# Optimization experiments

Hardware: AMD Instinct MI355X
Metric: run time of the kernel (lower is better)

Reference implementation:

```python
import jax, jax.numpy as jnp
import numpy as np

B, N = 16384, 32
OBS0, OBS1, OBS2 = 16, 64, 16
D = 64          # hidden dim / single_head_dim
H = 3           # n_heads
NACT = 2


def setup_inputs() -> dict:
    key = jax.random.key(0)
    ks = jax.random.split(key, 32)
    w = lambda i, shape: jax.random.normal(ks[i], shape, jnp.float32) * 0.05
    return {
        "s0": jax.random.normal(ks[0], (B, OBS0), jnp.float32),
        "s1": jax.random.normal(ks[1], (B, OBS1), jnp.float32),
        "s2": jax.random.normal(ks[2], (B, N, OBS2), jnp.float32),
        "W_own": w(3, (D, OBS0)), "b_own": w(4, (D,)),
        "W_env": w(5, (D, OBS1)), "b_env": w(6, (D,)),
        "W_s1": w(7, (D, OBS2)), "b_s1": w(8, (D,)),
        "W_s2": w(9, (D, D)),    "b_s2": w(10, (D,)),
        "W_q": w(11, (D, D)), "W_k": w(12, (D, D)), "W_v": w(13, (D, D)),
        "W_cq": w(14, (D, D)), "W_ck": w(15, (D, D)), "W_cv": w(16, (D, D)),
        "W_mo": w(17, (128, H * D)), "b_mo": w(18, (128,)),
        "W_a1": w(19, (64, 128)), "b_a1": w(20, (64,)),
        "W_a2": w(21, (NACT, 64)), "b_a2": w(22, (NACT,)),
    }


def reference(s0, s1, s2, W_own, b_own, W_env, b_env, W_s1, b_s1, W_s2, b_s2,
              W_q, W_k, W_v, W_cq, W_ck, W_cv, W_mo, b_mo, W_a1, b_a1, W_a2, b_a2):
    # branch encoders
    own_e = jax.nn.relu(s0 @ W_own.T + b_own)            # [B, 64]
    env_e = jax.nn.relu(s1 @ W_env.T + b_env)            # [B, 64]
    h = jax.nn.relu(s2 @ W_s1.T + b_s1)                  # [B, N, 64]
    intru_e = jax.nn.relu(h @ W_s2.T + b_s2)             # [B, N, 64]

    # masked single-head attention pooling over neighbors
    q = own_e @ W_q.T                                    # [B, 64]
    k = intru_e @ W_k.T                                  # [B, N, 64]
    v = intru_e @ W_v.T                                  # [B, N, 64]
    mask = jnp.mean(intru_e, axis=2, keepdims=True) != 0  # [B, N, 1] (bool of mean)
    score = jnp.einsum('bnd,bd->bn', k, q)[..., None]    # [B, N, 1]
    score = jnp.where(mask, score, -jnp.inf)
    alpha = jax.nn.softmax(score / np.sqrt(D).astype(np.float32), axis=1)
    alpha = jnp.where(mask, alpha, 0.0)
    v_att = jnp.sum(v * alpha, axis=1)                   # [B, 64]

    concat = jnp.concatenate([own_e, env_e, v_att], axis=1)  # [B, 192]

    # degenerate multi-head self-attention over seq_len=1
    b = concat.shape[0]
    raw = concat.reshape(b, 1, H, D)                     # [B, 1, H, D]
    comQ = (raw @ W_cq.T).transpose(0, 2, 1, 3)          # [B, H, 1, D]
    comK = (raw @ W_ck.T).transpose(0, 2, 1, 3)
    comV = (raw @ W_cv.T).transpose(0, 2, 1, 3)
    product = jnp.einsum('bhsd,bhtd->bhst', comQ, comK) / np.sqrt(D).astype(np.float32)
    attn = jax.nn.softmax(product, axis=-1)              # [B, H, 1, 1] == 1
    scores = attn @ comV                                 # [B, H, 1, D]
    concat_m = scores.transpose(0, 2, 1, 3).reshape(b, 1, H * D)  # [B, 1, 192]

    mo = concat_m @ W_mo.T + b_mo                        # [B, 1, 128]
    a = jax.nn.relu(mo @ W_a1.T + b_a1)                  # [B, 1, 64]
    return jnp.tanh(a @ W_a2.T + b_a2)                   # [B, 1, n_actions]
```

## Files before the change

### kernel.cpp

```cpp
#include <hip/hip_runtime.h>
#include <hip/hip_bf16.h>
#include <math.h>


typedef __attribute__((ext_vector_type(8))) short short8;
typedef __attribute__((ext_vector_type(4))) float f32x4;

#define WS_A1F   0
#define WS_A2F   1024
#define WS_AOWN  3072
#define WS_AENV  4096
#define WS_AQK   6144
#define WS_FOLDF 8192
#define WS_A1FR  20480
#define WS_SETUP_END 24576
#define WS_WCVV  24576
#define WS_WEND  28672

static __device__ inline unsigned pk2(float a, float b) {
    union { __hip_bfloat162 h; unsigned u; } cv;
    cv.h = __float22bfloat162_rn(make_float2(a, b));
    return cv.u;
}

__global__ void actor_wcvv(const float* __restrict__ wCv,
                           const float* __restrict__ wV,
                           float* __restrict__ ws)
{
    int t = blockIdx.x * 256 + threadIdx.x;
    int c = t >> 6, d = t & 63;
    float acc = 0.f;
    for (int e = 0; e < 64; ++e) acc = fmaf(wCv[c * 64 + e], wV[e * 64 + d], acc);
    ws[WS_WCVV + t] = acc;
}

__global__ void actor_setup(
    const float* __restrict__ wOwn, const float* __restrict__ wEnv,
    const float* __restrict__ wS1,  const float* __restrict__ wS2,
    const float* __restrict__ wQ,   const float* __restrict__ wK,
    const float* __restrict__ wCv,  const float* __restrict__ wMo,
    const float* __restrict__ wA1,  float* __restrict__ ws)
{
    int t = blockIdx.x * 256 + threadIdx.x;
    unsigned* wsu = reinterpret_cast<unsigned*>(ws);
    if (t < 1024) {
        int ht = t >> 8, rem = t & 255, lane = rem >> 2, jj = rem & 3;
        int qq = lane >> 4, m = lane & 15;
        int row = ht * 16 + m, k0 = qq * 8 + jj * 2;
        float v0 = (k0 < 16) ? wS1[row * 16 + k0]     : 0.f;
        float v1 = (k0 < 16) ? wS1[row * 16 + k0 + 1] : 0.f;
        wsu[WS_A1F + t] = pk2(v0, v1);
    } else if (t < 3072) {
        int u = t - 1024;
        int f = u >> 8, rem = u & 255, lane = rem >> 2, jj = rem & 3;
        int qq = lane >> 4, m = lane & 15;
        int dt = f >> 1, kt = f & 1;
        int row = dt * 16 + m, k = kt * 32 + qq * 8 + jj * 2;
        wsu[WS_A2F + u] = pk2(wS2[row * 64 + k], wS2[row * 64 + k + 1]);
    } else if (t < 4096) {
        int u = t - 3072;
        int ht = u >> 8, rem = u & 255, lane = rem >> 2, jj = rem & 3;
        int qq = lane >> 4, m = lane & 15;
        int row = ht * 16 + m, k0 = qq * 8 + jj * 2;
        float v0 = (k0 < 16) ? wOwn[row * 16 + k0]     : 0.f;
        float v1 = (k0 < 16) ? wOwn[row * 16 + k0 + 1] : 0.f;
        wsu[WS_AOWN + u] = pk2(v0, v1);
    } else if (t < 6144) {
        int u = t - 4096;
        int f = u >> 8, rem = u & 255, lane = rem >> 2, jj = rem & 3;
        int qq = lane >> 4, m = lane & 15;
        int ht = f >> 1, kt = f & 1;
        int row = ht * 16 + m, k = kt * 32 + qq * 8 + jj * 2;
        wsu[WS_AENV + u] = pk2(wEnv[row * 64 + k], wEnv[row * 64 + k + 1]);
    } else if (t < 8192) {
        int u = t - 6144;
        int f = u >> 8, rem = u & 255, lane = rem >> 2, jj = rem & 3;
        int qq = lane >> 4, m = lane & 15;
        int dt = f >> 1, kt = f & 1;
        int dp = dt * 16 + m;
        int e = kt * 32 + qq * 8 + jj * 2;
        float a0 = 0.f, a1 = 0.f;
        for (int d = 0; d < 64; ++d) {
            float kd = wK[d * 64 + dp];
            a0 = fmaf(wQ[d * 64 + e],     kd, a0);
            a1 = fmaf(wQ[d * 64 + e + 1], kd, a1);
        }
        wsu[WS_AQK + u] = pk2(a0, a1);
    } else if (t < 20480) {
        int u = t - 8192;
        int f = u >> 8, rem = u & 255, lane = rem >> 2, jj = rem & 3;
        int RT = f / 6, kt = f - RT * 6;
        int row = RT * 16 + (lane & 15);
        int k = kt * 32 + (lane >> 4) * 8 + jj * 2;
        int h = k >> 6, dp = k & 63;
        const float* wmr = wMo + row * 192 + h * 64;
        const float* rhs = (h == 2) ? (ws + WS_WCVV) : wCv;
        float a0 = 0.f, a1 = 0.f;
        for (int d = 0; d < 64; ++d) {
            float m = wmr[d];
            a0 = fmaf(m, rhs[d * 64 + dp],     a0);
            a1 = fmaf(m, rhs[d * 64 + dp + 1], a1);
        }
        wsu[WS_FOLDF + u] = pk2(a0, a1);
    } else if (t < WS_SETUP_END) {
        int u = t - 20480;
        int f = u >> 8, rem = u & 255, lane = rem >> 2, jj = rem & 3;
        int rt = f >> 2, kt = f & 3;
        int row = rt * 16 + (lane & 15);
        int k = kt * 32 + (lane >> 4) * 8 + jj * 2;
        wsu[WS_A1FR + u] = pk2(wA1[row * 128 + k], wA1[row * 128 + k + 1]);
    }
}

__global__ __launch_bounds__(256, 3) void actor_mega(
    const float* __restrict__ s0g, const float* __restrict__ s1g,
    const float* __restrict__ s2g,
    const float* __restrict__ bOwn, const float* __restrict__ bEnv,
    const float* __restrict__ bS1g, const float* __restrict__ bS2g,
    const float* __restrict__ bMo,  const float* __restrict__ bA1,
    const float* __restrict__ wA2,  const float* __restrict__ bA2,
    const float* __restrict__ ws,   float* __restrict__ outg)
{
    __shared__ char   xbL[16 * 384];
    __shared__ float  qkL[16][72];
    __shared__ ushort Hl[4][2][16 * 72];
    __shared__ ushort TR[16 * 72];
    __shared__ char   mbL[16 * 256];
    __shared__ float  aL[16][66];

    const int tid  = threadIdx.x;
    const int wid  = tid >> 6;
    const int lane = tid & 63;
    const int q    = lane >> 4;
    const int r    = lane & 15;
    const int swzr = (r & 7) << 4;
    const int eb   = blockIdx.x * 16;
    const f32x4 z = {0.f, 0.f, 0.f, 0.f};

    {
        short8 Ao = reinterpret_cast<const short8*>(ws + WS_AOWN)[wid * 64 + lane];
        const float* sp = s0g + (size_t)(eb + r) * 16 + (q & 1) * 8;
        float4 sa = *reinterpret_cast<const float4*>(sp);
        float4 sb = *reinterpret_cast<const float4*>(sp + 4);
        union { short8 s8; unsigned u[4]; } B;
        B.u[0] = pk2(sa.x, sa.y); B.u[1] = pk2(sa.z, sa.w);
        B.u[2] = pk2(sb.x, sb.y); B.u[3] = pk2(sb.z, sb.w);
        f32x4 c = *reinterpret_cast<const f32x4*>(bOwn + wid * 16 + q * 4);
        f32x4 D = __builtin_amdgcn_mfma_f32_16x16x32_bf16(Ao, B.s8, c, 0, 0, 0);
        unsigned p0 = pk2(fmaxf(D[0], 0.f), fmaxf(D[1], 0.f));
        unsigned p1 = pk2(fmaxf(D[2], 0.f), fmaxf(D[3], 0.f));
        *reinterpret_cast<uint2*>(xbL + r * 384 + ((wid * 32 + q * 8) ^ swzr)) =
            make_uint2(p0, p1);
        *reinterpret_cast<uint2*>(reinterpret_cast<char*>(TR) + r * 144 + wid * 32 + q * 8) =
            make_uint2(p0, p1);
    }
    {
        short8 Ae0 = reinterpret_cast<const short8*>(ws + WS_AENV)[(wid * 2 + 0) * 64 + lane];
        short8 Ae1 = reinterpret_cast<const short8*>(ws + WS_AENV)[(wid * 2 + 1) * 64 + lane];
        const float* sb1 = s1g + (size_t)(eb + r) * 64;
        f32x4 D = *reinterpret_cast<const f32x4*>(bEnv + wid * 16 + q * 4);
        {
            float4 sa = *reinterpret_cast<const float4*>(sb1 + q * 8);
            float4 sb = *reinterpret_cast<const float4*>(sb1 + q * 8 + 4);
            union { short8 s8; unsigned u[4]; } B;
            B.u[0] = pk2(sa.x, sa.y); B.u[1] = pk2(sa.z, sa.w);
            B.u[2] = pk2(sb.x, sb.y); B.u[3] = pk2(sb.z, sb.w);
            D = __builtin_amdgcn_mfma_f32_16x16x32_bf16(Ae0, B.s8, D, 0, 0, 0);
        }
        {
            float4 sa = *reinterpret_cast<const float4*>(sb1 + 32 + q * 8);
            float4 sb = *reinterpret_cast<const float4*>(sb1 + 32 + q * 8 + 4);
            union { short8 s8; unsigned u[4]; } B;
            B.u[0] = pk2(sa.x, sa.y); B.u[1] = pk2(sa.z, sa.w);
            B.u[2] = pk2(sb.x, sb.y); B.u[3] = pk2(sb.z, sb.w);
            D = __builtin_amdgcn_mfma_f32_16x16x32_bf16(Ae1, B.s8, D, 0, 0, 0);
        }
        unsigned p0 = pk2(fmaxf(D[0], 0.f), fmaxf(D[1], 0.f));
        unsigned p1 = pk2(fmaxf(D[2], 0.f), fmaxf(D[3], 0.f));
        *reinterpret_cast<uint2*>(xbL + r * 384 + ((128 + wid * 32 + q * 8) ^ swzr)) =
            make_uint2(p0, p1);
    }
    __syncthreads();

    {
        short8 Aq0 = reinterpret_cast<const short8*>(ws + WS_AQK)[(wid * 2 + 0) * 64 + lane];
        short8 Aq1 = reinterpret_cast<const short8*>(ws + WS_AQK)[(wid * 2 + 1) * 64 + lane];
        const char* trb = reinterpret_cast<const char*>(TR) + r * 144;
        short8 B0 = *reinterpret_cast<const short8*>(trb + q * 16);
        short8 B1 = *reinterpret_cast<const short8*>(trb + 64 + q * 16);
        f32x4 D = __builtin_amdgcn_mfma_f32_16x16x32_bf16(Aq0, B0, z, 0, 0, 0);
        D = __builtin_amdgcn_mfma_f32_16x16x32_bf16(Aq1, B1, D, 0, 0, 0);
        *reinterpret_cast<f32x4*>(&qkL[r][wid * 16 + q * 4]) = D;
    }
    __syncthreads();

    short8 A1[4], A2[8];
    {
        const short8* p1 = reinterpret_cast<const short8*>(ws + WS_A1F);
        #pragma unroll
        for (int ht = 0; ht < 4; ++ht) A1[ht] = p1[ht * 64 + lane];
        const short8* p2 = reinterpret_cast<const short8*>(ws + WS_A2F);
        #pragma unroll
        for (int f = 0; f < 8; ++f) A2[f] = p2[f * 64 + lane];
    }
    f32x4 b1c[4], b2c[4];
    #pragma unroll
    for (int t4 = 0; t4 < 4; ++t4) {
        b1c[t4] = *reinterpret_cast<const f32x4*>(bS1g + t4 * 16 + q * 4);
        b2c[t4] = *reinterpret_cast<const f32x4*>(bS2g + t4 * 16 + q * 4);
    }
    const int el   = r >> 2;
    const int j    = r & 3;
    const int sloc = wid * 4 + el;

    float qkf[16];
    #pragma unroll
    for (int dt = 0; dt < 4; ++dt) {
        f32x4 v = *reinterpret_cast<const f32x4*>(&qkL[sloc][dt * 16 + q * 4]);
        qkf[dt*4+0] = v[0]; qkf[dt*4+1] = v[1]; qkf[dt*4+2] = v[2]; qkf[dt*4+3] = v[3];
    }
    const float* s2base = s2g + (size_t)(eb + sloc) * 512 + (q & 1) * 8;

    float den = 0.f;
    f32x4 Pac[4] = {{0,0,0,0},{0,0,0,0},{0,0,0,0},{0,0,0,0}};

    #pragma unroll 2
    for (int it = 0; it < 8; ++it) {
        const float* sp = s2base + (it * 4 + j) * 16;
        float4 sa = *reinterpret_cast<const float4*>(sp);
        float4 sb = *reinterpret_cast<const float4*>(sp + 4);
        union { short8 s8; unsigned u[4]; } B1;
        B1.u[0] = pk2(sa.x, sa.y); B1.u[1] = pk2(sa.z, sa.w);
        B1.u[2] = pk2(sb.x, sb.y); B1.u[3] = pk2(sb.z, sb.w);

        f32x4 hD[4];
        #pragma unroll
        for (int ht = 0; ht < 4; ++ht)
            hD[ht] = __builtin_amdgcn_mfma_f32_16x16x32_bf16(A1[ht], B1.s8, b1c[ht], 0, 0, 0);

        ushort* hrow = &Hl[wid][it & 1][r * 72];
        #pragma unroll
        for (int ht = 0; ht < 4; ++ht) {
            float h0 = fmaxf(hD[ht][0], 0.f), h1 = fmaxf(hD[ht][1], 0.f);
            float h2 = fmaxf(hD[ht][2], 0.f), h3 = fmaxf(hD[ht][3], 0.f);
            *reinterpret_cast<uint2*>(hrow + ht * 16 + q * 4) =
                make_uint2(pk2(h0, h1), pk2(h2, h3));
        }
        short8 B2a = *reinterpret_cast<const short8*>(hrow + q * 8);
        short8 B2b = *reinterpret_cast<const short8*>(hrow + 32 + q * 8);

        f32x4 iD[4];
        #pragma unroll
        for (int dt = 0; dt < 4; ++dt) {
            f32x4 c0 = __builtin_amdgcn_mfma_f32_16x16x32_bf16(A2[dt*2+0], B2a, b2c[dt], 0, 0, 0);
            iD[dt]   = __builtin_amdgcn_mfma_f32_16x16x32_bf16(A2[dt*2+1], B2b, c0, 0, 0, 0);
        }
        float rs = 0.f, sc = 0.f;
        #pragma unroll
        for (int dt = 0; dt < 4; ++dt) {
            #pragma unroll
            for (int i = 0; i < 4; ++i) {
                float x = fmaxf(iD[dt][i], 0.f);
                iD[dt][i] = x;
                rs += x;
                sc = fmaf(x, qkf[dt*4+i], sc);
            }
        }
        sc += __shfl_xor(sc, 16, 64);
        sc += __shfl_xor(sc, 32, 64);
        rs += __shfl_xor(rs, 16, 64);
        rs += __shfl_xor(rs, 32, 64);
        float w = (rs != 0.f) ? __expf(sc * 0.125f) : 0.f;
        den += w;
        #pragma unroll
        for (int dt = 0; dt < 4; ++dt)
            #pragma unroll
            for (int i = 0; i < 4; ++i)
                Pac[dt][i] = fmaf(w, iD[dt][i], Pac[dt][i]);
    }
    #pragma unroll
    for (int m = 1; m <= 2; m <<= 1) {
        den += __shfl_xor(den, m, 64);
        #pragma unroll
        for (int dt = 0; dt < 4; ++dt)
            #pragma unroll
            for (int i = 0; i < 4; ++i)
                Pac[dt][i] += __shfl_xor(Pac[dt][i], m, 64);
    }
    {
        float inv = (den > 0.f) ? (1.f / den) : 0.f;
        if (j == 0) {
            const int swzs = (sloc & 7) << 4;
            #pragma unroll
            for (int dt = 0; dt < 4; ++dt) {
                float p0 = Pac[dt][0] * inv, p1 = Pac[dt][1] * inv;
                float p2 = Pac[dt][2] * inv, p3 = Pac[dt][3] * inv;
                *reinterpret_cast<uint2*>(xbL + sloc * 384 + ((256 + dt * 32 + q * 8) ^ swzs)) =
                    make_uint2(pk2(p0, p1), pk2(p2, p3));
            }
        }
    }
    __syncthreads();

    {
        const short8* fp = reinterpret_cast<const short8*>(ws + WS_FOLDF);
        short8 Amo0[6], Amo1[6];
        #pragma unroll
        for (int kt = 0; kt < 6; ++kt) {
            Amo0[kt] = fp[((wid * 2 + 0) * 6 + kt) * 64 + lane];
            Amo1[kt] = fp[((wid * 2 + 1) * 6 + kt) * 64 + lane];
        }
        short8 Bf[6];
        #pragma unroll
        for (int kt = 0; kt < 6; ++kt)
            Bf[kt] = *reinterpret_cast<const short8*>(
                xbL + r * 384 + ((kt * 64 + q * 16) ^ swzr));
        f32x4 D0 = z, D1 = z;
        #pragma unroll
        for (int kt = 0; kt < 6; ++kt) {
            D0 = __builtin_amdgcn_mfma_f32_16x16x32_bf16(Amo0[kt], Bf[kt], D0, 0, 0, 0);
            D1 = __builtin_amdgcn_mfma_f32_16x16x32_bf16(Amo1[kt], Bf[kt], D1, 0, 0, 0);
        }
        f32x4 bm0 = *reinterpret_cast<const f32x4*>(bMo + wid * 32 + q * 4);
        f32x4 bm1 = *reinterpret_cast<const f32x4*>(bMo + wid * 32 + 16 + q * 4);
        char* wp0 = mbL + r * 256 + ((wid * 64 + q * 8) ^ swzr);
        *reinterpret_cast<unsigned*>(wp0)     = pk2(D0[0] + bm0[0], D0[1] + bm0[1]);
        *reinterpret_cast<unsigned*>(wp0 + 4) = pk2(D0[2] + bm0[2], D0[3] + bm0[3]);
        char* wp1 = mbL + r * 256 + ((wid * 64 + 32 + q * 8) ^ swzr);
        *reinterpret_cast<unsigned*>(wp1)     = pk2(D1[0] + bm1[0], D1[1] + bm1[1]);
        *reinterpret_cast<unsigned*>(wp1 + 4) = pk2(D1[2] + bm1[2], D1[3] + bm1[3]);
    }
    __syncthreads();

    {
        const short8* ap = reinterpret_cast<const short8*>(ws + WS_A1FR);
        f32x4 D = z;
        #pragma unroll
        for (int kt = 0; kt < 4; ++kt) {
            short8 Ak = ap[(wid * 4 + kt) * 64 + lane];
            short8 Bk = *reinterpret_cast<const short8*>(
                mbL + r * 256 + ((kt * 64 + q * 16) ^ swzr));
            D = __builtin_amdgcn_mfma_f32_16x16x32_bf16(Ak, Bk, D, 0, 0, 0);
        }
        f32x4 ba = *reinterpret_cast<const f32x4*>(bA1 + wid * 16 + q * 4);
        float a0 = fmaxf(D[0] + ba[0], 0.f), a1v = fmaxf(D[1] + ba[1], 0.f);
        float a2v = fmaxf(D[2] + ba[2], 0.f), a3v = fmaxf(D[3] + ba[3], 0.f);
        *reinterpret_cast<float2*>(&aL[r][wid * 16 + q * 4])     = make_float2(a0, a1v);
        *reinterpret_cast<float2*>(&aL[r][wid * 16 + q * 4 + 2]) = make_float2(a2v, a3v);
    }
    __syncthreads();

    if (tid < 32) {
        const int s = tid & 15, o = tid >> 4;
        const float* wr = wA2 + o * 64;
        float p = 0.f;
        #pragma unroll
        for (int d = 0; d < 64; ++d) p = fmaf(aL[s][d], wr[d], p);
        outg[(size_t)(eb + s) * 2 + o] = tanhf(p + bA2[o]);
    }
}

extern "C" void kernel_launch(void* const* d_in, const int* in_sizes, int n_in,
                              void* d_out, int out_size, void* d_ws, size_t ws_size,
                              hipStream_t stream) {
    const float* s0   = (const float*)d_in[0];
    const float* s1   = (const float*)d_in[1];
    const float* s2   = (const float*)d_in[2];
    const float* wOwn = (const float*)d_in[3];
    const float* bOwn = (const float*)d_in[4];
    const float* wEnv = (const float*)d_in[5];
    const float* bEnv = (const float*)d_in[6];
    const float* wS1  = (const float*)d_in[7];
    const float* bS1  = (const float*)d_in[8];
    const float* wS2  = (const float*)d_in[9];
    const float* bS2  = (const float*)d_in[10];
    const float* wQ   = (const float*)d_in[11];
    const float* wK   = (const float*)d_in[12];
    const float* wV   = (const float*)d_in[13];
    const float* wCv  = (const float*)d_in[16];
    const float* wMo  = (const float*)d_in[17];
    const float* bMo  = (const float*)d_in[18];
    const float* wA1  = (const float*)d_in[19];
    const float* bA1  = (const float*)d_in[20];
    const float* wA2  = (const float*)d_in[21];
    const float* bA2  = (const float*)d_in[22];
    float* ws  = (float*)d_ws;
    float* out = (float*)d_out;

    hipLaunchKernelGGL(actor_wcvv, dim3(16), dim3(256), 0, stream, wCv, wV, ws);
    hipLaunchKernelGGL(actor_setup, dim3(WS_SETUP_END / 256), dim3(256), 0, stream,
                       wOwn, wEnv, wS1, wS2, wQ, wK, wCv, wMo, wA1, ws);
    hipLaunchKernelGGL(actor_mega, dim3(16384 / 16), dim3(256), 0, stream,
                       s0, s1, s2, bOwn, bEnv, bS1, bS2, bMo, bA1, wA2, bA2,
                       ws, out);
}
```

Baseline: 40.25 us.

## Split setup into pack/gemm kernels, fold biases into MFMA, shrink LDS for occupancy

Setup weight-folding GEMMs now split each dot product across 8 lanes with shuffle reductions and run in a separate, wider kernel, which shortens the serial setup chain. The own and s1 biases are folded into the MFMA A fragments as an extra K column fed by a constant 1.0 input. Shared memory is merged into one aliased pool and qk is stored as bf16, raising launch bounds to 4 blocks per CU. This trades a small amount of precision and an extra kernel launch for more occupancy and a shorter setup.

```diff
diff --git a/kernel.cpp b/kernel.cpp
--- a/kernel.cpp
+++ b/kernel.cpp
@@ -15,12 +15,17 @@
 #define WS_A1FR  20480
 #define WS_SETUP_END 24576
 #define WS_WCVV  24576
-#define WS_WEND  28672
 
 static __device__ inline unsigned pk2(float a, float b) {
     union { __hip_bfloat162 h; unsigned u; } cv;
     cv.h = __float22bfloat162_rn(make_float2(a, b));
     return cv.u;
+}
+static __device__ inline float bflo(unsigned u) {
+    union { unsigned x; float f; } c; c.x = u << 16; return c.f;
+}
+static __device__ inline float bfhi(unsigned u) {
+    union { unsigned x; float f; } c; c.x = u & 0xffff0000u; return c.f;
 }
 
 __global__ void actor_wcvv(const float* __restrict__ wCv,
@@ -28,17 +33,24 @@
                            float* __restrict__ ws)
 {
     int t = blockIdx.x * 256 + threadIdx.x;
-    int c = t >> 6, d = t & 63;
+    int out = t >> 3, sl = t & 7;
+    int c = out >> 6, d = out & 63;
     float acc = 0.f;
-    for (int e = 0; e < 64; ++e) acc = fmaf(wCv[c * 64 + e], wV[e * 64 + d], acc);
-    ws[WS_WCVV + t] = acc;
-}
-
-__global__ void actor_setup(
-    const float* __restrict__ wOwn, const float* __restrict__ wEnv,
-    const float* __restrict__ wS1,  const float* __restrict__ wS2,
-    const float* __restrict__ wQ,   const float* __restrict__ wK,
-    const float* __restrict__ wCv,  const float* __restrict__ wMo,
+    #pragma unroll
+    for (int i = 0; i < 8; ++i) {
+        int e = sl * 8 + i;
+        acc = fmaf(wCv[c * 64 + e], wV[e * 64 + d], acc);
+    }
+    acc += __shfl_xor(acc, 1, 64);
+    acc += __shfl_xor(acc, 2, 64);
+    acc += __shfl_xor(acc, 4, 64);
+    if (sl == 0) ws[WS_WCVV + out] = acc;
+}
+
+__global__ void actor_setup_pack(
+    const float* __restrict__ wOwn, const float* __restrict__ bOwn,
+    const float* __restrict__ wEnv, const float* __restrict__ wS1,
+    const float* __restrict__ bS1,  const float* __restrict__ wS2,
     const float* __restrict__ wA1,  float* __restrict__ ws)
 {
     int t = blockIdx.x * 256 + threadIdx.x;
@@ -47,8 +59,8 @@
         int ht = t >> 8, rem = t & 255, lane = rem >> 2, jj = rem & 3;
         int qq = lane >> 4, m = lane & 15;
         int row = ht * 16 + m, k0 = qq * 8 + jj * 2;
-        float v0 = (k0 < 16) ? wS1[row * 16 + k0]     : 0.f;
-        float v1 = (k0 < 16) ? wS1[row * 16 + k0 + 1] : 0.f;
+        float v0 = (k0 < 16) ? wS1[row * 16 + k0] : (k0 == 16 ? bS1[row] : 0.f);
+        float v1 = (k0 + 1 < 16) ? wS1[row * 16 + k0 + 1] : 0.f;
         wsu[WS_A1F + t] = pk2(v0, v1);
     } else if (t < 3072) {
         int u = t - 1024;
@@ -62,8 +74,8 @@
         int ht = u >> 8, rem = u & 255, lane = rem >> 2, jj = rem & 3;
         int qq = lane >> 4, m = lane & 15;
         int row = ht * 16 + m, k0 = qq * 8 + jj * 2;
-        float v0 = (k0 < 16) ? wOwn[row * 16 + k0]     : 0.f;
-        float v1 = (k0 < 16) ? wOwn[row * 16 + k0 + 1] : 0.f;
+        float v0 = (k0 < 16) ? wOwn[row * 16 + k0] : (k0 == 16 ? bOwn[row] : 0.f);
+        float v1 = (k0 + 1 < 16) ? wOwn[row * 16 + k0 + 1] : 0.f;
         wsu[WS_AOWN + u] = pk2(v0, v1);
     } else if (t < 6144) {
         int u = t - 4096;
@@ -72,22 +84,25 @@
         int ht = f >> 1, kt = f & 1;
         int row = ht * 16 + m, k = kt * 32 + qq * 8 + jj * 2;
         wsu[WS_AENV + u] = pk2(wEnv[row * 64 + k], wEnv[row * 64 + k + 1]);
-    } else if (t < 8192) {
+    } else {
         int u = t - 6144;
         int f = u >> 8, rem = u & 255, lane = rem >> 2, jj = rem & 3;
-        int qq = lane >> 4, m = lane & 15;
-        int dt = f >> 1, kt = f & 1;
-        int dp = dt * 16 + m;
-        int e = kt * 32 + qq * 8 + jj * 2;
-        float a0 = 0.f, a1 = 0.f;
-        for (int d = 0; d < 64; ++d) {
-            float kd = wK[d * 64 + dp];
-            a0 = fmaf(wQ[d * 64 + e],     kd, a0);
-            a1 = fmaf(wQ[d * 64 + e + 1], kd, a1);
-        }
-        wsu[WS_AQK + u] = pk2(a0, a1);
-    } else if (t < 20480) {
-        int u = t - 8192;
+        int rt = f >> 2, kt = f & 3;
+        int row = rt * 16 + (lane & 15);
+        int k = kt * 32 + (lane >> 4) * 8 + jj * 2;
+        wsu[WS_A1FR + u] = pk2(wA1[row * 128 + k], wA1[row * 128 + k + 1]);
+    }
+}
+
+__global__ void actor_setup_gemm(
+    const float* __restrict__ wQ,  const float* __restrict__ wK,
+    const float* __restrict__ wCv, const float* __restrict__ wMo,
+    float* __restrict__ ws)
+{
+    int t = blockIdx.x * 256 + threadIdx.x;
+    unsigned* wsu = reinterpret_cast<unsigned*>(ws);
+    if (t < 98304) {
+        int u = t >> 3, sl = t & 7;
         int f = u >> 8, rem = u & 255, lane = rem >> 2, jj = rem & 3;
         int RT = f / 6, kt = f - RT * 6;
         int row = RT * 16 + (lane & 15);
@@ -96,37 +111,50 @@
         const float* wmr = wMo + row * 192 + h * 64;
         const float* rhs = (h == 2) ? (ws + WS_WCVV) : wCv;
         float a0 = 0.f, a1 = 0.f;
-        for (int d = 0; d < 64; ++d) {
+        #pragma unroll
+        for (int i = 0; i < 8; ++i) {
+            int d = sl * 8 + i;
             float m = wmr[d];
             a0 = fmaf(m, rhs[d * 64 + dp],     a0);
             a1 = fmaf(m, rhs[d * 64 + dp + 1], a1);
         }
-        wsu[WS_FOLDF + u] = pk2(a0, a1);
-    } else if (t < WS_SETUP_END) {
-        int u = t - 20480;
+        a0 += __shfl_xor(a0, 1, 64); a0 += __shfl_xor(a0, 2, 64); a0 += __shfl_xor(a0, 4, 64);
+        a1 += __shfl_xor(a1, 1, 64); a1 += __shfl_xor(a1, 2, 64); a1 += __shfl_xor(a1, 4, 64);
+        if (sl == 0) wsu[WS_FOLDF + u] = pk2(a0, a1);
+    } else {
+        int v = t - 98304;
+        int u = v >> 3, sl = v & 7;
         int f = u >> 8, rem = u & 255, lane = rem >> 2, jj = rem & 3;
-        int rt = f >> 2, kt = f & 3;
-        int row = rt * 16 + (lane & 15);
-        int k = kt * 32 + (lane >> 4) * 8 + jj * 2;
-        wsu[WS_A1FR + u] = pk2(wA1[row * 128 + k], wA1[row * 128 + k + 1]);
-    }
-}
-
-__global__ __launch_bounds__(256, 3) void actor_mega(
+        int qq = lane >> 4, m = lane & 15;
+        int dt = f >> 1, kt = f & 1;
+        int dp = dt * 16 + m;
+        int e = kt * 32 + qq * 8 + jj * 2;
+        float a0 = 0.f, a1 = 0.f;
+        #pragma unroll
+        for (int i = 0; i < 8; ++i) {
+            int d = sl * 8 + i;
+            float kd = wK[d * 64 + dp];
+            a0 = fmaf(wQ[d * 64 + e],     kd, a0);
+            a1 = fmaf(wQ[d * 64 + e + 1], kd, a1);
+        }
+        a0 += __shfl_xor(a0, 1, 64); a0 += __shfl_xor(a0, 2, 64); a0 += __shfl_xor(a0, 4, 64);
+        a1 += __shfl_xor(a1, 1, 64); a1 += __shfl_xor(a1, 2, 64); a1 += __shfl_xor(a1, 4, 64);
+        if (sl == 0) wsu[WS_AQK + u] = pk2(a0, a1);
+    }
+}
+
+__global__ __launch_bounds__(256, 4) void actor_mega(
     const float* __restrict__ s0g, const float* __restrict__ s1g,
     const float* __restrict__ s2g,
-    const float* __restrict__ bOwn, const float* __restrict__ bEnv,
-    const float* __restrict__ bS1g, const float* __restrict__ bS2g,
+    const float* __restrict__ bEnv, const float* __restrict__ bS2g,
     const float* __restrict__ bMo,  const float* __restrict__ bA1,
     const float* __restrict__ wA2,  const float* __restrict__ bA2,
     const float* __restrict__ ws,   float* __restrict__ outg)
 {
-    __shared__ char   xbL[16 * 384];
-    __shared__ float  qkL[16][72];
-    __shared__ ushort Hl[4][2][16 * 72];
-    __shared__ ushort TR[16 * 72];
-    __shared__ char   mbL[16 * 256];
-    __shared__ float  aL[16][66];
+    __shared__ __align__(16) char pool[27136];
+    char*     xbL     = pool;
+    unsigned* qkL     = reinterpret_cast<unsigned*>(pool + 6144);
+    char*     scratch = pool + 8704;
 
     const int tid  = threadIdx.x;
     const int wid  = tid >> 6;
@@ -139,19 +167,23 @@
 
     {
         short8 Ao = reinterpret_cast<const short8*>(ws + WS_AOWN)[wid * 64 + lane];
-        const float* sp = s0g + (size_t)(eb + r) * 16 + (q & 1) * 8;
-        float4 sa = *reinterpret_cast<const float4*>(sp);
-        float4 sb = *reinterpret_cast<const float4*>(sp + 4);
         union { short8 s8; unsigned u[4]; } B;
-        B.u[0] = pk2(sa.x, sa.y); B.u[1] = pk2(sa.z, sa.w);
-        B.u[2] = pk2(sb.x, sb.y); B.u[3] = pk2(sb.z, sb.w);
-        f32x4 c = *reinterpret_cast<const f32x4*>(bOwn + wid * 16 + q * 4);
-        f32x4 D = __builtin_amdgcn_mfma_f32_16x16x32_bf16(Ao, B.s8, c, 0, 0, 0);
+        if (q < 2) {
+            const float* sp = s0g + (size_t)(eb + r) * 16 + q * 8;
+            float4 sa = *reinterpret_cast<const float4*>(sp);
+            float4 sb = *reinterpret_cast<const float4*>(sp + 4);
+            B.u[0] = pk2(sa.x, sa.y); B.u[1] = pk2(sa.z, sa.w);
+            B.u[2] = pk2(sb.x, sb.y); B.u[3] = pk2(sb.z, sb.w);
+        } else {
+            B.u[0] = (q == 2) ? 0x00003f80u : 0u;
+            B.u[1] = 0u; B.u[2] = 0u; B.u[3] = 0u;
+        }
+        f32x4 D = __builtin_amdgcn_mfma_f32_16x16x32_bf16(Ao, B.s8, z, 0, 0, 0);
         unsigned p0 = pk2(fmaxf(D[0], 0.f), fmaxf(D[1], 0.f));
         unsigned p1 = pk2(fmaxf(D[2], 0.f), fmaxf(D[3], 0.f));
         *reinterpret_cast<uint2*>(xbL + r * 384 + ((wid * 32 + q * 8) ^ swzr)) =
             make_uint2(p0, p1);
-        *reinterpret_cast<uint2*>(reinterpret_cast<char*>(TR) + r * 144 + wid * 32 + q * 8) =
+        *reinterpret_cast<uint2*>(scratch + r * 144 + wid * 32 + q * 8) =
             make_uint2(p0, p1);
     }
     {
@@ -185,12 +217,13 @@
     {
         short8 Aq0 = reinterpret_cast<const short8*>(ws + WS_AQK)[(wid * 2 + 0) * 64 + lane];
         short8 Aq1 = reinterpret_cast<const short8*>(ws + WS_AQK)[(wid * 2 + 1) * 64 + lane];
-        const char* trb = reinterpret_cast<const char*>(TR) + r * 144;
+        const char* trb = scratch + r * 144;
         short8 B0 = *reinterpret_cast<const short8*>(trb + q * 16);
         short8 B1 = *reinterpret_cast<const short8*>(trb + 64 + q * 16);
         f32x4 D = __builtin_amdgcn_mfma_f32_16x16x32_bf16(Aq0, B0, z, 0, 0, 0);
         D = __builtin_amdgcn_mfma_f32_16x16x32_bf16(Aq1, B1, D, 0, 0, 0);
-        *reinterpret_cast<f32x4*>(&qkL[r][wid * 16 + q * 4]) = D;
+        *reinterpret_cast<uint2*>(qkL + r * 40 + wid * 8 + q * 2) =
+            make_uint2(pk2(D[0], D[1]), pk2(D[2], D[3]));
     }
     __syncthreads();
 
@@ -203,42 +236,50 @@
         #pragma unroll
         for (int f = 0; f < 8; ++f) A2[f] = p2[f * 64 + lane];
     }
-    f32x4 b1c[4], b2c[4];
+    f32x4 b2c[4];
     #pragma unroll
-    for (int t4 = 0; t4 < 4; ++t4) {
-        b1c[t4] = *reinterpret_cast<const f32x4*>(bS1g + t4 * 16 + q * 4);
+    for (int t4 = 0; t4 < 4; ++t4)
         b2c[t4] = *reinterpret_cast<const f32x4*>(bS2g + t4 * 16 + q * 4);
-    }
+
     const int el   = r >> 2;
     const int j    = r & 3;
     const int sloc = wid * 4 + el;
 
-    float qkf[16];
-    #pragma unroll
-    for (int dt = 0; dt < 4; ++dt) {
-        f32x4 v = *reinterpret_cast<const f32x4*>(&qkL[sloc][dt * 16 + q * 4]);
-        qkf[dt*4+0] = v[0]; qkf[dt*4+1] = v[1]; qkf[dt*4+2] = v[2]; qkf[dt*4+3] = v[3];
-    }
-    const float* s2base = s2g + (size_t)(eb + sloc) * 512 + (q & 1) * 8;
+    unsigned qkp[8];
+    {
+        const unsigned* qp = qkL + sloc * 40;
+        #pragma unroll
+        for (int dt = 0; dt < 4; ++dt) {
+            uint2 v = *reinterpret_cast<const uint2*>(qp + dt * 8 + q * 2);
+            qkp[dt * 2] = v.x; qkp[dt * 2 + 1] = v.y;
+        }
+    }
+    const float* s2base = s2g + (size_t)(eb + sloc) * 512 + q * 8;
 
     float den = 0.f;
     f32x4 Pac[4] = {{0,0,0,0},{0,0,0,0},{0,0,0,0},{0,0,0,0}};
 
     #pragma unroll 2
     for (int it = 0; it < 8; ++it) {
-        const float* sp = s2base + (it * 4 + j) * 16;
-        float4 sa = *reinterpret_cast<const float4*>(sp);
-        float4 sb = *reinterpret_cast<const float4*>(sp + 4);
         union { short8 s8; unsigned u[4]; } B1;
-        B1.u[0] = pk2(sa.x, sa.y); B1.u[1] = pk2(sa.z, sa.w);
-        B1.u[2] = pk2(sb.x, sb.y); B1.u[3] = pk2(sb.z, sb.w);
+        if (q < 2) {
+            const float* sp = s2base + (it * 4 + j) * 16;
+            float4 sa = *reinterpret_cast<const float4*>(sp);
+            float4 sb = *reinterpret_cast<const float4*>(sp + 4);
+            B1.u[0] = pk2(sa.x, sa.y); B1.u[1] = pk2(sa.z, sa.w);
+            B1.u[2] = pk2(sb.x, sb.y); B1.u[3] = pk2(sb.z, sb.w);
+        } else {
+            B1.u[0] = (q == 2) ? 0x00003f80u : 0u;
+            B1.u[1] = 0u; B1.u[2] = 0u; B1.u[3] = 0u;
+        }
 
         f32x4 hD[4];
         #pragma unroll
         for (int ht = 0; ht < 4; ++ht)
-            hD[ht] = __builtin_amdgcn_mfma_f32_16x16x32_bf16(A1[ht], B1.s8, b1c[ht], 0, 0, 0);
-
-        ushort* hrow = &Hl[wid][it & 1][r * 72];
+            hD[ht] = __builtin_amdgcn_mfma_f32_16x16x32_bf16(A1[ht], B1.s8, z, 0, 0, 0);
+
+        ushort* hrow = reinterpret_cast<ushort*>(
+            scratch + (wid * 2 + (it & 1)) * 2304) + r * 72;
         #pragma unroll
         for (int ht = 0; ht < 4; ++ht) {
             float h0 = fmaxf(hD[ht][0], 0.f), h1 = fmaxf(hD[ht][1], 0.f);
@@ -258,13 +299,14 @@
         float rs = 0.f, sc = 0.f;
         #pragma unroll
         for (int dt = 0; dt < 4; ++dt) {
-            #pragma unroll
-            for (int i = 0; i < 4; ++i) {
-                float x = fmaxf(iD[dt][i], 0.f);
-                iD[dt][i] = x;
-                rs += x;
-                sc = fmaf(x, qkf[dt*4+i], sc);
-            }
+            float x0 = fmaxf(iD[dt][0], 0.f), x1 = fmaxf(iD[dt][1], 0.f);
+            float x2 = fmaxf(iD[dt][2], 0.f), x3 = fmaxf(iD[dt][3], 0.f);
+            iD[dt][0] = x0; iD[dt][1] = x1; iD[dt][2] = x2; iD[dt][3] = x3;
+            rs += (x0 + x1) + (x2 + x3);
+            sc = fmaf(x0, bflo(qkp[dt*2]),     sc);
+            sc = fmaf(x1, bfhi(qkp[dt*2]),     sc);
+            sc = fmaf(x2, bflo(qkp[dt*2+1]),   sc);
+            sc = fmaf(x3, bfhi(qkp[dt*2+1]),   sc);
         }
         sc += __shfl_xor(sc, 16, 64);
         sc += __shfl_xor(sc, 32, 64);
@@ -302,6 +344,9 @@
     }
     __syncthreads();
 
+    char*  mbL = scratch;
+    float* aL  = reinterpret_cast<float*>(scratch + 4096);
+
     {
         const short8* fp = reinterpret_cast<const short8*>(ws + WS_FOLDF);
         short8 Amo0[6], Amo1[6];
@@ -345,8 +390,8 @@
         f32x4 ba = *reinterpret_cast<const f32x4*>(bA1 + wid * 16 + q * 4);
         float a0 = fmaxf(D[0] + ba[0], 0.f), a1v = fmaxf(D[1] + ba[1], 0.f);
         float a2v = fmaxf(D[2] + ba[2], 0.f), a3v = fmaxf(D[3] + ba[3], 0.f);
-        *reinterpret_cast<float2*>(&aL[r][wid * 16 + q * 4])     = make_float2(a0, a1v);
-        *reinterpret_cast<float2*>(&aL[r][wid * 16 + q * 4 + 2]) = make_float2(a2v, a3v);
+        *reinterpret_cast<float2*>(aL + r * 66 + wid * 16 + q * 4)     = make_float2(a0, a1v);
+        *reinterpret_cast<float2*>(aL + r * 66 + wid * 16 + q * 4 + 2) = make_float2(a2v, a3v);
     }
     __syncthreads();
 
@@ -355,7 +400,7 @@
         const float* wr = wA2 + o * 64;
         float p = 0.f;
         #pragma unroll
-        for (int d = 0; d < 64; ++d) p = fmaf(aL[s][d], wr[d], p);
+        for (int d = 0; d < 64; ++d) p = fmaf(aL[s * 66 + d], wr[d], p);
         outg[(size_t)(eb + s) * 2 + o] = tanhf(p + bA2[o]);
     }
 }
@@ -387,10 +432,11 @@
     float* ws  = (float*)d_ws;
     float* out = (float*)d_out;
 
-    hipLaunchKernelGGL(actor_wcvv, dim3(16), dim3(256), 0, stream, wCv, wV, ws);
-    hipLaunchKernelGGL(actor_setup, dim3(WS_SETUP_END / 256), dim3(256), 0, stream,
-                       wOwn, wEnv, wS1, wS2, wQ, wK, wCv, wMo, wA1, ws);
+    hipLaunchKernelGGL(actor_wcvv, dim3(128), dim3(256), 0, stream, wCv, wV, ws);
+    hipLaunchKernelGGL(actor_setup_pack, dim3(40), dim3(256), 0, stream,
+                       wOwn, bOwn, wEnv, wS1, bS1, wS2, wA1, ws);
+    hipLaunchKernelGGL(actor_setup_gemm, dim3(448), dim3(256), 0, stream,
+                       wQ, wK, wCv, wMo, ws);
     hipLaunchKernelGGL(actor_mega, dim3(16384 / 16), dim3(256), 0, stream,
-                       s0, s1, s2, bOwn, bEnv, bS1, bS2, bMo, bA1, wA2, bA2,
-                       ws, out);
-}
+                       s0, s1, s2, bEnv, bS2, bMo, bA1, wA2, bA2, ws, out);
+}
```

New measurement: 47.07 us. 1.17x slower.
